# Optimization experiments

Hardware: AMD Instinct MI355X
Metric: run time of the kernel (lower is better)

Reference implementation:

```python
import jax, jax.numpy as jnp
import numpy as np

B, OBS, ACT, NT, E, H1, H2, D = 4096, 390, 20, 10, 8, 1024, 512, 256


def setup_inputs() -> dict:
    key = jax.random.key(0)
    ks = jax.random.split(key, 16)
    f32 = jnp.float32

    def w(k, shape, fan_in):
        return jax.random.normal(k, shape, f32) / np.float32(np.sqrt(fan_in))

    return {
        "state_feat": jax.random.normal(ks[0], (B, OBS), f32),
        "act": jax.random.normal(ks[1], (B, ACT), f32),
        "task_id": jax.random.randint(ks[2], (B,), 0, NT, jnp.int32),
        "rep_W1": w(ks[3], (OBS + ACT, H1), OBS + ACT),
        "rep_b1": jnp.zeros((H1,), f32),
        "rep_W2": w(ks[4], (H1, H1), H1),
        "rep_b2": jnp.zeros((H1,), f32),
        "emb": 0.5 * jax.random.normal(ks[5], (NT, D), f32),
        "kW1": w(ks[6], (E, H1, H2), H1),
        "kb1": jnp.zeros((E, H2), f32),
        "kW2": w(ks[7], (E, H2, D), H2),
        "kb2": jnp.zeros((E, D), f32),
        "vW1": w(ks[8], (E, H1, H2), H1),
        "vb1": jnp.zeros((E, H2), f32),
        "vW2": w(ks[9], (E, H2, D), H2),
        "vb2": jnp.zeros((E, D), f32),
        "tW1": w(ks[10], (D, D), D),
        "tb1": jnp.zeros((D,), f32),
        "tW2": w(ks[11], (D, D), D),
        "tb2": jnp.zeros((D,), f32),
        "tW3": w(ks[12], (D, 1), D),
        "tb3": jnp.zeros((1,), f32),
    }


def reference(state_feat, act, task_id, rep_W1, rep_b1, rep_W2, rep_b2, emb,
              kW1, kb1, kW2, kb2, vW1, vb1, vW2, vb2,
              tW1, tb1, tW2, tb2, tW3, tb3):
    # representation: mlp([obs+act, 1024, 1024]) -> ReLU on first layer only
    x = jnp.concatenate([state_feat, act], axis=-1)              # [B, 410]
    rep = jnp.maximum(x @ rep_W1 + rep_b1, 0.0) @ rep_W2 + rep_b2  # [B, H1]
    query = jnp.tanh(emb[task_id])                               # [B, D]

    # batched per-expert key/value MLPs (grouped GEMM instead of python loop)
    hk = jnp.maximum(jnp.einsum('bi,eio->ebo', rep, kW1) + kb1[:, None, :], 0.0)
    keys = jnp.einsum('ebo,eod->ebd', hk, kW2) + kb2[:, None, :]   # [E, B, D]
    hv = jnp.maximum(jnp.einsum('bi,eio->ebo', rep, vW1) + vb1[:, None, :], 0.0)
    vals = jnp.einsum('ebo,eod->ebd', hv, vW2) + vb2[:, None, :]   # [E, B, D]

    scores = jnp.einsum('bd,ebd->be', query, keys)               # [B, E]
    weight = jax.nn.softmax(scores, axis=1)                      # [B, E]
    tower_in = jnp.einsum('be,ebd->bd', weight, vals)            # [B, D]

    # tower: mlp([256, 256, 256, 1]) -> ReLU, ReLU, Identity
    h = jnp.maximum(tower_in @ tW1 + tb1, 0.0)
    h = jnp.maximum(h @ tW2 + tb2, 0.0)
    q = (h @ tW3 + tb3)[:, 0]                                    # [B]

    expert_loss = -jnp.mean(
        jnp.sum(jnp.clip(jnp.log(weight + 1e-10), -6.0, 0.0), axis=-1) * 0.3)
    return q, expert_loss
```

## Files before the change

kernel.cpp:

```cpp
#include <hip/hip_runtime.h>

constexpr int Bn   = 4096;
constexpr int OBS  = 390;
constexpr int ACTN = 20;
constexpr int IN   = 410;
constexpr int KPAD = 448;
constexpr int E    = 8;
constexpr int NT   = 10;
constexpr int H1   = 1024;
constexpr int H2   = 512;
constexpr int D    = 256;

typedef __bf16 bf16x8 __attribute__((ext_vector_type(8)));
typedef float  f32x4  __attribute__((ext_vector_type(4)));
typedef unsigned short u16x8 __attribute__((ext_vector_type(8)));

__device__ __forceinline__ unsigned short f2bf(float f) {
    unsigned int u = __float_as_uint(f);
    unsigned int r = u + 0x7fffu + ((u >> 16) & 1u);
    return (unsigned short)(r >> 16);
}
__device__ __forceinline__ float bf2f(unsigned short h) {
    return __uint_as_float(((unsigned int)h) << 16);
}
__device__ __forceinline__ void gload16(void* lds_dst, const void* g_src) {
    __builtin_amdgcn_global_load_lds(
        (const __attribute__((address_space(1))) void*)g_src,
        (__attribute__((address_space(3))) void*)lds_dst,
        16, 0, 0);
}

struct TD2 {
    const float* W;
    unsigned short* WT;
    int K, Kpad, N;
    long long gsW, gsO;
    int tilesN, perG, start;
};
struct TD2Arr { TD2 d[8]; };

__global__ __launch_bounds__(256) void tc64(TD2Arr da) {
    int bid = blockIdx.x;
    int i = 0;
#pragma unroll
    for (int j = 1; j < 8; ++j) if (bid >= da.d[j].start) i = j;
    TD2 dd = da.d[i];
    int local = bid - dd.start;
    int g   = local / dd.perG;
    int rem = local - g * dd.perG;
    int kt  = rem / dd.tilesN;
    int nt  = rem - kt * dd.tilesN;
    const float* W = dd.W + (long long)g * dd.gsW;
    unsigned short* WT = dd.WT + (long long)g * dd.gsO;
    int k0 = kt * 64, n0 = nt * 64;

    __shared__ float tile[64][68];
    int t = threadIdx.x;
    {
        int kl  = t >> 4;
        int nl4 = (t & 15) * 4;
#pragma unroll
        for (int r = 0; r < 4; ++r) {
            int k = k0 + kl + r * 16;
            float4 v = make_float4(0.f, 0.f, 0.f, 0.f);
            if (k < dd.K) v = *(const float4*)(W + (long long)k * dd.N + n0 + nl4);
            *(float4*)&tile[kl + r * 16][nl4] = v;
        }
    }
    __syncthreads();
    int nl = t >> 2, kc = (t & 3) * 16;
    if (k0 + kc < dd.Kpad) {
        u16x8 o0, o1;
#pragma unroll
        for (int j = 0; j < 8; ++j) {
            o0[j] = f2bf(tile[kc + j][nl]);
            o1[j] = f2bf(tile[kc + 8 + j][nl]);
        }
        unsigned short* dst = WT + (long long)(n0 + nl) * dd.Kpad + k0 + kc;
        *(u16x8*)dst       = o0;
        *(u16x8*)(dst + 8) = o1;
    }
}

constexpr int PREPB = (Bn * KPAD) / 256;

__global__ __launch_bounds__(256) void misc_kernel(
    const float* __restrict__ sf, const float* __restrict__ ac,
    unsigned short* __restrict__ x,
    const float* __restrict__ kW2, const float* __restrict__ kb2,
    const float* __restrict__ emb, float* __restrict__ qp, float* __restrict__ qb,
    const float* __restrict__ kb1, const float* __restrict__ vb1,
    float* __restrict__ b1cat)
{
    int bid = blockIdx.x;
    if (bid < PREPB) {
        int idx = bid * 256 + threadIdx.x;
        int b = idx / KPAD;
        int k = idx - b * KPAD;
        float v = 0.f;
        if (k < OBS) v = sf[b * OBS + k];
        else if (k < IN) v = ac[b * ACTN + (k - OBS)];
        x[idx] = f2bf(v);
        return;
    }
    if (bid < PREPB + 17) {
        int qbid = bid - PREPB;
        __shared__ float tq[NT][D];
        for (int i = threadIdx.x; i < NT * D; i += 256)
            tq[i / D][i - (i / D) * D] = tanhf(emb[i]);
        __syncthreads();
        if (qbid < 16) {
            int e = qbid >> 1;
            int h = (qbid & 1) * 256 + threadIdx.x;
            const float4* row = (const float4*)(kW2 + ((long long)e * H2 + h) * D);
            float acc[NT] = {};
            for (int d4 = 0; d4 < D / 4; ++d4) {
                float4 wv = row[d4];
#pragma unroll
                for (int t = 0; t < NT; ++t)
                    acc[t] += wv.x * tq[t][d4 * 4] + wv.y * tq[t][d4 * 4 + 1]
                            + wv.z * tq[t][d4 * 4 + 2] + wv.w * tq[t][d4 * 4 + 3];
            }
#pragma unroll
            for (int t = 0; t < NT; ++t)
                qp[((long long)e * NT + t) * H2 + h] = acc[t];
        } else if (threadIdx.x < E * NT) {
            int e = threadIdx.x / NT, t = threadIdx.x - e * NT;
            float s = 0.f;
            for (int d = 0; d < D; ++d) s += kb2[e * D + d] * tq[t][d];
            qb[e * NT + t] = s;
        }
        return;
    }
    int i = (bid - PREPB - 17) * 256 + threadIdx.x;
    b1cat[i] = (i < E * H2) ? kb1[i] : vb1[i - E * H2];
}

template <int KT, int ACTF, int OUTF>
__global__ __launch_bounds__(256, 2) void gemm128p(
    const unsigned short* __restrict__ A, const unsigned short* __restrict__ BT,
    const float* __restrict__ bias, void* __restrict__ Cout,
    int ldc, long long gsA, long long gsBT, long long gsBias, long long gsC,
    const float* __restrict__ tW3 = nullptr, float* __restrict__ qpart = nullptr)
{
    constexpr int NTK = KT / 64;
    static_assert(NTK >= 2, "KT must be >= 128");

    const int g = blockIdx.z;
    A    += (long long)g * gsA;
    BT   += (long long)g * gsBT;
    bias += (long long)g * gsBias;
    float*          Cf = (float*)Cout + (long long)g * gsC;
    unsigned short* Cb = (unsigned short*)Cout + (long long)g * gsC;

    __shared__ __align__(16) char smem[65536];
    const int tid = threadIdx.x;
    const int l  = tid & 63, lr = l & 15, lk = l >> 4;
    const int w  = tid >> 6;
    const int wm = (w >> 1) * 64, wn = (w & 1) * 64;
    const int gm = blockIdx.y * 128, gn = blockIdx.x * 128;

    const int srow = tid >> 3;
    const int cg   = (tid & 7) ^ (srow & 7);
    const unsigned short* gA = A  + (long long)(gm + srow) * KT + cg * 8;
    const unsigned short* gB = BT + (long long)(gn + srow) * KT + cg * 8;
    const int wb = w * 1024;

    const int cs0 = ((0 | lk) ^ (lr & 7)) * 16;
    const int cs1 = ((4 | lk) ^ (lr & 7)) * 16;
    const int aRow = (wm + lr) * 128;
    const int bRow = 16384 + (wn + lr) * 128;

    f32x4 acc[4][4] = {};

    auto stA = [&](int c, int kt) {
#pragma unroll
        for (int j = 0; j < 4; ++j)
            gload16(smem + c * 32768 + j * 4096 + wb,
                    gA + (long long)(j * 32) * KT + kt * 64);
    };
    auto stB = [&](int c, int kt) {
#pragma unroll
        for (int j = 0; j < 4; ++j)
            gload16(smem + c * 32768 + 16384 + j * 4096 + wb,
                    gB + (long long)(j * 32) * KT + kt * 64);
    };

    stA(0, 0); stB(0, 0); stA(1, 1);
    asm volatile("s_waitcnt vmcnt(4)" ::: "memory");
    __builtin_amdgcn_s_barrier();
    __builtin_amdgcn_sched_barrier(0);

#pragma unroll
    for (int kt = 0; kt < NTK; ++kt) {
        const int c = kt & 1;
        const char* bufc = smem + c * 32768;
        bf16x8 a[4][2], b[2][2], b2[2][2];

#pragma unroll
        for (int m = 0; m < 4; ++m) {
            const char* base = bufc + aRow + m * 2048;
            a[m][0] = *(const bf16x8*)(base + cs0);
            a[m][1] = *(const bf16x8*)(base + cs1);
        }
#pragma unroll
        for (int n = 0; n < 2; ++n) {
            const char* base = bufc + bRow + n * 2048;
            b[n][0] = *(const bf16x8*)(base + cs0);
            b[n][1] = *(const bf16x8*)(base + cs1);
        }
        if (kt + 1 < NTK) stB(c ^ 1, kt + 1);
        __builtin_amdgcn_s_setprio(1);
#pragma unroll
        for (int ks = 0; ks < 2; ++ks)
#pragma unroll
            for (int m = 0; m < 4; ++m)
#pragma unroll
                for (int n = 0; n < 2; ++n)
                    acc[m][n] = __builtin_amdgcn_mfma_f32_16x16x32_bf16(
                        a[m][ks], b[n][ks], acc[m][n], 0, 0, 0);
        __builtin_amdgcn_s_setprio(0);

#pragma unroll
        for (int n = 0; n < 2; ++n) {
            const char* base = bufc + bRow + (2 + n) * 2048;
            b2[n][0] = *(const bf16x8*)(base + cs0);
            b2[n][1] = *(const bf16x8*)(base + cs1);
        }
        asm volatile("s_waitcnt lgkmcnt(0)" ::: "memory");
        __builtin_amdgcn_sched_barrier(0);
        if (kt + 2 < NTK) {
            __builtin_amdgcn_s_barrier();
            __builtin_amdgcn_sched_barrier(0);
            stA(c, kt + 2);
        }
        __builtin_amdgcn_s_setprio(1);
#pragma unroll
        for (int ks = 0; ks < 2; ++ks)
#pragma unroll
            for (int m = 0; m < 4; ++m)
#pragma unroll
                for (int n = 0; n < 2; ++n)
                    acc[m][2 + n] = __builtin_amdgcn_mfma_f32_16x16x32_bf16(
                        a[m][ks], b2[n][ks], acc[m][2 + n], 0, 0, 0);
        __builtin_amdgcn_s_setprio(0);

        if (kt + 1 < NTK) {
            if (kt + 2 < NTK) { asm volatile("s_waitcnt vmcnt(4)" ::: "memory"); }
            else              { asm volatile("s_waitcnt vmcnt(0)" ::: "memory"); }
            __builtin_amdgcn_sched_barrier(0);
            __builtin_amdgcn_s_barrier();
            __builtin_amdgcn_sched_barrier(0);
        }
    }

    const int orow0 = gm + wm + lk * 4;
    const int ocol0 = gn + wn + lr;
    float bv[4];
#pragma unroll
    for (int ni = 0; ni < 4; ++ni) bv[ni] = bias[gn + wn + lr + ni * 16];

    if (OUTF == 2) {
        float tw3v[4];
#pragma unroll
        for (int ni = 0; ni < 4; ++ni) tw3v[ni] = tW3[gn + wn + lr + ni * 16];
#pragma unroll
        for (int mi = 0; mi < 4; ++mi)
#pragma unroll
            for (int r = 0; r < 4; ++r) {
                float part = 0.f;
#pragma unroll
                for (int ni = 0; ni < 4; ++ni) {
                    float v = acc[mi][ni][r] + bv[ni];
                    if (ACTF == 1) v = fmaxf(v, 0.f);
                    part += v * tw3v[ni];
                }
                part += __shfl_xor(part, 1);
                part += __shfl_xor(part, 2);
                part += __shfl_xor(part, 4);
                part += __shfl_xor(part, 8);
                if (lr == 0)
                    qpart[(orow0 + mi * 16 + r) * 4 + ((wn >> 6) << 1) + blockIdx.x] = part;
            }
    } else {
#pragma unroll
        for (int mi = 0; mi < 4; ++mi)
#pragma unroll
            for (int ni = 0; ni < 4; ++ni)
#pragma unroll
                for (int r = 0; r < 4; ++r) {
                    float v = acc[mi][ni][r] + bv[ni];
                    if (ACTF == 1) v = fmaxf(v, 0.f);
                    long long off = (long long)(orow0 + mi * 16 + r) * ldc + ocol0 + ni * 16;
                    if (OUTF == 0) Cf[off] = v;
                    else           Cb[off] = f2bf(v);
                }
    }
}

template <int KTOT, int ACTF, int OUTF, int SC>
__global__ __launch_bounds__(512, 2) void gemm256(
    const unsigned short* __restrict__ A, const unsigned short* __restrict__ BT,
    const float* __restrict__ bias, void* __restrict__ Cout,
    int ldc, long long gsA, long long gsBT, long long gsBias, long long gsC,
    const int* __restrict__ task_id, const float* __restrict__ qp,
    float* __restrict__ spart)
{
    constexpr int NT_ = KTOT / 64;
    static_assert(NT_ >= 4 && (NT_ % 2) == 0, "KTOT must be multiple of 128");

    const int g = blockIdx.z;
    A    += (long long)g * gsA;
    BT   += (long long)g * gsBT;
    bias += (long long)g * gsBias;
    float*          Cf = (float*)Cout + (long long)g * gsC;
    unsigned short* Cb = (unsigned short*)Cout + (long long)g * gsC;

    __shared__ __align__(16) char smem[131072];

    const int tid = threadIdx.x;
    const int l  = tid & 63;
    const int lr = l & 15, lk = l >> 4;
    const int w  = tid >> 6;
    const int wr = w >> 2, wc = w & 3;
    const int gm = blockIdx.y * 256, gn = blockIdx.x * 256;

    const int srow = tid >> 3;
    const int cg   = (tid & 7) ^ (srow & 7);
    const unsigned short* gA = A  + (long long)(gm + srow) * KTOT + cg * 8;
    const unsigned short* gB = BT + (long long)(gn + srow) * KTOT + cg * 8;
    const int wbase = (tid & ~63) * 16;

    const int cs0 = ((0 | lk) ^ (lr & 7)) * 16;
    const int cs1 = ((4 | lk) ^ (lr & 7)) * 16;
    const int aRow = wr * 16384 + lr * 128;
    const int bRow = 32768 + (wc >> 1) * 16384 + ((wc & 1) * 64 + lr) * 128;

    f32x4 acc[8][4] = {};

    auto stA = [&](int c, int s, int kt) {
        const unsigned short* src = gA + (long long)(s * 128) * KTOT + kt * 64;
        char* d = smem + c * 65536 + s * 16384 + wbase;
        gload16(d,        src);
        gload16(d + 8192, src + (long long)64 * KTOT);
    };
    auto stB = [&](int c, int s, int kt) {
        const unsigned short* src = gB + (long long)(s * 128) * KTOT + kt * 64;
        char* d = smem + c * 65536 + 32768 + s * 16384 + wbase;
        gload16(d,        src);
        gload16(d + 8192, src + (long long)64 * KTOT);
    };

    stA(0, 0, 0); stA(0, 1, 0); stB(0, 0, 0); stB(0, 1, 0);
    stA(1, 0, 1); stA(1, 1, 1);
    asm volatile("s_waitcnt vmcnt(4)" ::: "memory");
    __builtin_amdgcn_s_barrier();
    __builtin_amdgcn_sched_barrier(0);

#pragma unroll
    for (int kt = 0; kt < NT_; ++kt) {
        const int c = kt & 1;
        const char* bufc = smem + c * 65536;
        bf16x8 a0[4], a1[4], b0[4], b1[4];

#pragma unroll
        for (int m = 0; m < 4; ++m) {
            const char* base = bufc + aRow + m * (16 * 128);
            a0[m] = *(const bf16x8*)(base + cs0);
            a1[m] = *(const bf16x8*)(base + cs1);
        }
#pragma unroll
        for (int n = 0; n < 4; ++n) {
            const char* base = bufc + bRow + n * (16 * 128);
            b0[n] = *(const bf16x8*)(base + cs0);
            b1[n] = *(const bf16x8*)(base + cs1);
        }
        if (kt + 1 < NT_) { stB(c ^ 1, 0, kt + 1); stB(c ^ 1, 1, kt + 1); }
        __builtin_amdgcn_s_setprio(1);
#pragma unroll
        for (int m = 0; m < 4; ++m)
#pragma unroll
            for (int n = 0; n < 4; ++n) {
                acc[m][n] = __builtin_amdgcn_mfma_f32_16x16x32_bf16(a0[m], b0[n], acc[m][n], 0, 0, 0);
                acc[m][n] = __builtin_amdgcn_mfma_f32_16x16x32_bf16(a1[m], b1[n], acc[m][n], 0, 0, 0);
            }
        __builtin_amdgcn_s_setprio(0);

#pragma unroll
        for (int m = 0; m < 4; ++m) {
            const char* base = bufc + aRow + (64 + m * 16) * 128;
            a0[m] = *(const bf16x8*)(base + cs0);
            a1[m] = *(const bf16x8*)(base + cs1);
        }
        asm volatile("s_waitcnt lgkmcnt(0)" ::: "memory");
        __builtin_amdgcn_sched_barrier(0);
        if (kt + 2 < NT_) {
            __builtin_amdgcn_s_barrier();
            __builtin_amdgcn_sched_barrier(0);
            stA(c, 0, kt + 2); stA(c, 1, kt + 2);
        }
        __builtin_amdgcn_s_setprio(1);
#pragma unroll
        for (int m = 0; m < 4; ++m)
#pragma unroll
            for (int n = 0; n < 4; ++n) {
                acc[4 + m][n] = __builtin_amdgcn_mfma_f32_16x16x32_bf16(a0[m], b0[n], acc[4 + m][n], 0, 0, 0);
                acc[4 + m][n] = __builtin_amdgcn_mfma_f32_16x16x32_bf16(a1[m], b1[n], acc[4 + m][n], 0, 0, 0);
            }
        __builtin_amdgcn_s_setprio(0);

        if (kt + 1 < NT_) {
            if (kt + 2 < NT_) { asm volatile("s_waitcnt vmcnt(4)" ::: "memory"); }
            else              { asm volatile("s_waitcnt vmcnt(0)" ::: "memory"); }
            __builtin_amdgcn_sched_barrier(0);
            __builtin_amdgcn_s_barrier();
            __builtin_amdgcn_sched_barrier(0);
        }
    }

    const int orow0 = gm + wr * 128 + lk * 4;
    const int ocol0 = gn + wc * 64 + lr;
    float bv[4];
#pragma unroll
    for (int ni = 0; ni < 4; ++ni) bv[ni] = bias[gn + wc * 64 + lr + ni * 16];

    if (SC && g < E) {
        __syncthreads();
        float* qpl  = (float*)smem;
        int*   tidl = (int*)(smem + NT * 256 * 4);
        for (int i = tid; i < NT * 256; i += 512) {
            int tt = i >> 8, cc = i & 255;
            qpl[i] = qp[((long long)(g * NT + tt)) * H2 + gn + cc];
        }
        if (tid < 256) tidl[tid] = task_id[gm + tid];
        __syncthreads();

        const int rbase = wr * 128 + lk * 4;
        const int cbase = wc * 64 + lr;
#pragma unroll
        for (int mi = 0; mi < 8; ++mi) {
#pragma unroll
            for (int r = 0; r < 4; ++r) {
                int trow = tidl[rbase + mi * 16 + r];
                float rp = 0.f;
#pragma unroll
                for (int ni = 0; ni < 4; ++ni) {
                    float v = acc[mi][ni][r] + bv[ni];
                    v = fmaxf(v, 0.f);
                    rp += v * qpl[trow * 256 + cbase + ni * 16];
                }
                rp += __shfl_xor(rp, 1);
                rp += __shfl_xor(rp, 2);
                rp += __shfl_xor(rp, 4);
                rp += __shfl_xor(rp, 8);
                if (lr == 0)
                    spart[(((long long)g * Bn + orow0 + mi * 16 + r) << 3)
                          + (wc << 1) + blockIdx.x] = rp;
            }
        }
    } else {
#pragma unroll
        for (int mi = 0; mi < 8; ++mi)
#pragma unroll
            for (int ni = 0; ni < 4; ++ni)
#pragma unroll
                for (int r = 0; r < 4; ++r) {
                    float v = acc[mi][ni][r] + bv[ni];
                    if (ACTF == 1) v = fmaxf(v, 0.f);
                    long long off = (long long)(orow0 + mi * 16 + r) * ldc + ocol0 + ni * 16;
                    if (OUTF == 0) Cf[off] = v;
                    else           Cb[off] = f2bf(v);
                }
    }
}

__global__ __launch_bounds__(256) void attn_kernel(
    const float* __restrict__ spart, const float* __restrict__ qb,
    const int* __restrict__ task_id, const unsigned short* __restrict__ vals,
    unsigned short* __restrict__ tower_in, float* __restrict__ loss_partial)
{
    int wv   = threadIdx.x >> 6;
    int lane = threadIdx.x & 63;
    int b    = blockIdx.x * 4 + wv;
    int t    = task_id[b];

    float s[E];
#pragma unroll
    for (int e = 0; e < E; ++e) {
        const float4* sp = (const float4*)(spart + (((long long)e * Bn + b) << 3));
        float4 p0 = sp[0], p1 = sp[1];
        s[e] = p0.x + p0.y + p0.z + p0.w + p1.x + p1.y + p1.z + p1.w + qb[e * NT + t];
    }

    float m = s[0];
#pragma unroll
    for (int e = 1; e < E; ++e) m = fmaxf(m, s[e]);
    float wgt[E];
    float sum = 0.f;
#pragma unroll
    for (int e = 0; e < E; ++e) { wgt[e] = expf(s[e] - m); sum += wgt[e]; }
    float inv = 1.f / sum;

    int d0 = lane * 4;
    float4 acc = make_float4(0.f, 0.f, 0.f, 0.f);
    float lb = 0.f;
#pragma unroll
    for (int e = 0; e < E; ++e) {
        float we = wgt[e] * inv;
        uint2 vv = *(const uint2*)&vals[((long long)e * Bn + b) * D + d0];
        acc.x += we * __uint_as_float(vv.x << 16);
        acc.y += we * __uint_as_float(vv.x & 0xffff0000u);
        acc.z += we * __uint_as_float(vv.y << 16);
        acc.w += we * __uint_as_float(vv.y & 0xffff0000u);
        lb += fminf(fmaxf(logf(we + 1e-10f), -6.f), 0.f);
    }
    ushort4 o;
    o.x = f2bf(acc.x); o.y = f2bf(acc.y); o.z = f2bf(acc.z); o.w = f2bf(acc.w);
    *(ushort4*)&tower_in[(long long)b * D + d0] = o;

    __shared__ float sm[4];
    if (lane == 0) sm[wv] = lb;
    __syncthreads();
    if (threadIdx.x == 0)
        loss_partial[blockIdx.x] = sm[0] + sm[1] + sm[2] + sm[3];
}

__global__ __launch_bounds__(256) void qfin_kernel(
    const float* __restrict__ qpart, const float* __restrict__ tb3,
    float* __restrict__ out, const float* __restrict__ lossp)
{
    if (blockIdx.x == Bn / 256) {
        float s = 0.f;
        for (int i = threadIdx.x; i < Bn / 4; i += 256) s += lossp[i];
#pragma unroll
        for (int off = 32; off > 0; off >>= 1) s += __shfl_xor(s, off, 64);
        __shared__ float sm[4];
        if ((threadIdx.x & 63) == 0) sm[threadIdx.x >> 6] = s;
        __syncthreads();
        if (threadIdx.x == 0) out[Bn] = (-0.3f / Bn) * (sm[0] + sm[1] + sm[2] + sm[3]);
        return;
    }
    int b = blockIdx.x * 256 + threadIdx.x;
    float4 qpv = *(const float4*)&qpart[b * 4];
    out[b] = qpv.x + qpv.y + qpv.z + qpv.w + tb3[0];
}

extern "C" void kernel_launch(void* const* d_in, const int* in_sizes, int n_in,
                              void* d_out, int out_size, void* d_ws, size_t ws_size,
                              hipStream_t stream) {
    const float* state_feat = (const float*)d_in[0];
    const float* act        = (const float*)d_in[1];
    const int*   task_id    = (const int*)d_in[2];
    const float* rep_W1 = (const float*)d_in[3];
    const float* rep_b1 = (const float*)d_in[4];
    const float* rep_W2 = (const float*)d_in[5];
    const float* rep_b2 = (const float*)d_in[6];
    const float* emb    = (const float*)d_in[7];
    const float* kW1 = (const float*)d_in[8];
    const float* kb1 = (const float*)d_in[9];
    const float* kW2 = (const float*)d_in[10];
    const float* kb2 = (const float*)d_in[11];
    const float* vW1 = (const float*)d_in[12];
    const float* vb1 = (const float*)d_in[13];
    const float* vW2 = (const float*)d_in[14];
    const float* vb2 = (const float*)d_in[15];
    const float* tW1 = (const float*)d_in[16];
    const float* tb1 = (const float*)d_in[17];
    const float* tW2 = (const float*)d_in[18];
    const float* tb2 = (const float*)d_in[19];
    const float* tW3 = (const float*)d_in[20];
    const float* tb3 = (const float*)d_in[21];
    float* out = (float*)d_out;

    char* p = (char*)d_ws;
    auto alloc = [&](size_t bytes) {
        char* r = p;
        p += (bytes + 255) & ~(size_t)255;
        return r;
    };
    unsigned short* x      = (unsigned short*)alloc((size_t)Bn * KPAD * 2);
    unsigned short* repW1T = (unsigned short*)alloc((size_t)H1 * KPAD * 2);
    unsigned short* repW2T = (unsigned short*)alloc((size_t)H1 * H1 * 2);
    unsigned short* w1T    = (unsigned short*)alloc((size_t)2 * E * H2 * H1 * 2);
    unsigned short* w2T    = (unsigned short*)alloc((size_t)E * D * H2 * 2);
    unsigned short* tW1T   = (unsigned short*)alloc((size_t)D * D * 2);
    unsigned short* tW2T   = (unsigned short*)alloc((size_t)D * D * 2);
    float*          b1cat  = (float*)alloc((size_t)2 * E * H2 * 4);
    float*          qp     = (float*)alloc((size_t)E * NT * H2 * 4);
    float*          qb     = (float*)alloc((size_t)E * NT * 4);
    char*           h1zone = alloc((size_t)Bn * H1 * 2);
    unsigned short* rep    = (unsigned short*)alloc((size_t)Bn * H1 * 2);
    unsigned short* hkv    = (unsigned short*)alloc((size_t)2 * E * Bn * H2 * 2);
    unsigned short* vals   = (unsigned short*)alloc((size_t)E * Bn * D * 2);
    float*          spart  = (float*)alloc((size_t)E * Bn * 8 * 4);
    float*          qpart  = (float*)alloc((size_t)Bn * 4 * 4);
    float*          lossp  = (float*)alloc((size_t)(Bn / 4) * 4);

    unsigned short* h1       = (unsigned short*)h1zone;
    unsigned short* tower_in = (unsigned short*)h1zone;
    unsigned short* t1       = (unsigned short*)(h1zone + (size_t)Bn * D * 2);
    unsigned short* hv = hkv + (size_t)E * Bn * H2;

    TD2Arr da;
    int startAcc = 0;
    auto setd = [&](int i, const float* W, unsigned short* WT, int K, int Kpad, int N,
                    long long gsW, long long gsO, int groups) {
        TD2& dd = da.d[i];
        dd.W = W; dd.WT = WT; dd.K = K; dd.Kpad = Kpad; dd.N = N;
        dd.gsW = gsW; dd.gsO = gsO;
        dd.tilesN = N / 64;
        dd.perG = ((Kpad + 63) / 64) * dd.tilesN;
        dd.start = startAcc;
        startAcc += dd.perG * groups;
    };
    setd(0, rep_W1, repW1T, IN, KPAD, H1, 0, 0, 1);
    setd(1, rep_W2, repW2T, H1, H1, H1, 0, 0, 1);
    setd(2, kW1, w1T,                       H1, H1, H2, (long long)H1 * H2, (long long)H2 * H1, E);
    setd(3, vW1, w1T + (size_t)E * H2 * H1, H1, H1, H2, (long long)H1 * H2, (long long)H2 * H1, E);
    setd(4, vW2, w2T,                       H2, H2, D, (long long)H2 * D, (long long)D * H2, E);
    setd(5, tW1, tW1T, D, D, D, 0, 0, 1);
    setd(6, tW2, tW2T, D, D, D, 0, 0, 1);
    da.d[7] = da.d[6];
    da.d[7].start = 0x7fffffff;
    tc64<<<startAcc, 256, 0, stream>>>(da);

    misc_kernel<<<PREPB + 17 + 32, 256, 0, stream>>>(
        state_feat, act, x, kW2, kb2, emb, qp, qb, kb1, vb1, b1cat);

    gemm128p<KPAD, 1, 1><<<dim3(H1 / 128, Bn / 128, 1), 256, 0, stream>>>(
        x, repW1T, rep_b1, h1, H1, 0, 0, 0, 0);
    gemm128p<H1, 0, 1><<<dim3(H1 / 128, Bn / 128, 1), 256, 0, stream>>>(
        h1, repW2T, rep_b2, rep, H1, 0, 0, 0, 0);

    gemm256<H1, 1, 1, 1><<<dim3(H2 / 256, Bn / 256, 2 * E), 512, 0, stream>>>(
        rep, w1T, b1cat, hkv, H2,
        0, (long long)H2 * H1, H2, (long long)Bn * H2,
        task_id, qp, spart);
    gemm128p<H2, 0, 1><<<dim3(D / 128, Bn / 128, E), 256, 0, stream>>>(
        hv, w2T, vb2, vals, D,
        (long long)Bn * H2, (long long)D * H2, D, (long long)Bn * D);

    attn_kernel<<<Bn / 4, 256, 0, stream>>>(
        spart, qb, task_id, vals, tower_in, lossp);

    gemm128p<D, 1, 1><<<dim3(D / 128, Bn / 128, 1), 256, 0, stream>>>(
        tower_in, tW1T, tb1, t1, D, 0, 0, 0, 0);
    gemm128p<D, 1, 2><<<dim3(D / 128, Bn / 128, 1), 256, 0, stream>>>(
        t1, tW2T, tb2, nullptr, D, 0, 0, 0, 0, tW3, qpart);

    qfin_kernel<<<Bn / 256 + 1, 256, 0, stream>>>(qpart, tb3, out, lossp);
}
```

Before: 162.3 us.

## Restructure GEMM main loop into four A-subtile phases with interleaved prefetch

The k-loop of the grouped GEMM is split into four phases, each loading two 16-row A fragments and issuing their MFMAs, while B fragments are held in registers for the whole k-tile. Prefetch order is swapped: B is now staged one tile ahead and A is loaded into the alternate buffer in halves across phases. Smaller A register sets are meant to cut register pressure and spread global loads more evenly between MFMA bursts. The cost is many more workgroup barriers per iteration, which could stall waves.

```diff
diff --git a/kernel.cpp b/kernel.cpp
--- a/kernel.cpp
+++ b/kernel.cpp
@@ -352,7 +352,7 @@
     };
 
     stA(0, 0, 0); stA(0, 1, 0); stB(0, 0, 0); stB(0, 1, 0);
-    stA(1, 0, 1); stA(1, 1, 1);
+    stB(1, 0, 1); stB(1, 1, 1);
     asm volatile("s_waitcnt vmcnt(4)" ::: "memory");
     __builtin_amdgcn_s_barrier();
     __builtin_amdgcn_sched_barrier(0);
@@ -361,61 +361,107 @@
     for (int kt = 0; kt < NT_; ++kt) {
         const int c = kt & 1;
         const char* bufc = smem + c * 65536;
-        bf16x8 a0[4], a1[4], b0[4], b1[4];
-
-#pragma unroll
-        for (int m = 0; m < 4; ++m) {
-            const char* base = bufc + aRow + m * (16 * 128);
-            a0[m] = *(const bf16x8*)(base + cs0);
-            a1[m] = *(const bf16x8*)(base + cs1);
-        }
+        bf16x8 b[4][2], ap[2][2];
+
 #pragma unroll
         for (int n = 0; n < 4; ++n) {
-            const char* base = bufc + bRow + n * (16 * 128);
-            b0[n] = *(const bf16x8*)(base + cs0);
-            b1[n] = *(const bf16x8*)(base + cs1);
-        }
-        if (kt + 1 < NT_) { stB(c ^ 1, 0, kt + 1); stB(c ^ 1, 1, kt + 1); }
-        __builtin_amdgcn_s_setprio(1);
-#pragma unroll
-        for (int m = 0; m < 4; ++m)
-#pragma unroll
-            for (int n = 0; n < 4; ++n) {
-                acc[m][n] = __builtin_amdgcn_mfma_f32_16x16x32_bf16(a0[m], b0[n], acc[m][n], 0, 0, 0);
-                acc[m][n] = __builtin_amdgcn_mfma_f32_16x16x32_bf16(a1[m], b1[n], acc[m][n], 0, 0, 0);
-            }
-        __builtin_amdgcn_s_setprio(0);
-
-#pragma unroll
-        for (int m = 0; m < 4; ++m) {
-            const char* base = bufc + aRow + (64 + m * 16) * 128;
-            a0[m] = *(const bf16x8*)(base + cs0);
-            a1[m] = *(const bf16x8*)(base + cs1);
-        }
+            const char* base = bufc + bRow + n * 2048;
+            b[n][0] = *(const bf16x8*)(base + cs0);
+            b[n][1] = *(const bf16x8*)(base + cs1);
+        }
+#pragma unroll
+        for (int m = 0; m < 2; ++m) {
+            const char* base = bufc + aRow + m * 2048;
+            ap[m][0] = *(const bf16x8*)(base + cs0);
+            ap[m][1] = *(const bf16x8*)(base + cs1);
+        }
+        if (kt + 1 < NT_) stA(c ^ 1, 0, kt + 1);
+        __builtin_amdgcn_s_barrier();
         asm volatile("s_waitcnt lgkmcnt(0)" ::: "memory");
         __builtin_amdgcn_sched_barrier(0);
-        if (kt + 2 < NT_) {
-            __builtin_amdgcn_s_barrier();
-            __builtin_amdgcn_sched_barrier(0);
-            stA(c, 0, kt + 2); stA(c, 1, kt + 2);
-        }
         __builtin_amdgcn_s_setprio(1);
 #pragma unroll
-        for (int m = 0; m < 4; ++m)
-#pragma unroll
-            for (int n = 0; n < 4; ++n) {
-                acc[4 + m][n] = __builtin_amdgcn_mfma_f32_16x16x32_bf16(a0[m], b0[n], acc[4 + m][n], 0, 0, 0);
-                acc[4 + m][n] = __builtin_amdgcn_mfma_f32_16x16x32_bf16(a1[m], b1[n], acc[4 + m][n], 0, 0, 0);
-            }
+        for (int ks = 0; ks < 2; ++ks)
+#pragma unroll
+            for (int m = 0; m < 2; ++m)
+#pragma unroll
+                for (int n = 0; n < 4; ++n)
+                    acc[m][n] = __builtin_amdgcn_mfma_f32_16x16x32_bf16(
+                        ap[m][ks], b[n][ks], acc[m][n], 0, 0, 0);
         __builtin_amdgcn_s_setprio(0);
-
+        __builtin_amdgcn_s_barrier();
+
+#pragma unroll
+        for (int m = 0; m < 2; ++m) {
+            const char* base = bufc + aRow + 4096 + m * 2048;
+            ap[m][0] = *(const bf16x8*)(base + cs0);
+            ap[m][1] = *(const bf16x8*)(base + cs1);
+        }
+        if (kt + 1 < NT_) stA(c ^ 1, 1, kt + 1);
+        __builtin_amdgcn_s_barrier();
+        asm volatile("s_waitcnt lgkmcnt(0)" ::: "memory");
+        __builtin_amdgcn_sched_barrier(0);
+        __builtin_amdgcn_s_setprio(1);
+#pragma unroll
+        for (int ks = 0; ks < 2; ++ks)
+#pragma unroll
+            for (int m = 0; m < 2; ++m)
+#pragma unroll
+                for (int n = 0; n < 4; ++n)
+                    acc[2 + m][n] = __builtin_amdgcn_mfma_f32_16x16x32_bf16(
+                        ap[m][ks], b[n][ks], acc[2 + m][n], 0, 0, 0);
+        __builtin_amdgcn_s_setprio(0);
+        __builtin_amdgcn_s_barrier();
+
+#pragma unroll
+        for (int m = 0; m < 2; ++m) {
+            const char* base = bufc + aRow + 8192 + m * 2048;
+            ap[m][0] = *(const bf16x8*)(base + cs0);
+            ap[m][1] = *(const bf16x8*)(base + cs1);
+        }
+        if (kt + 2 < NT_) stB(c, 0, kt + 2);
+        __builtin_amdgcn_s_barrier();
+        asm volatile("s_waitcnt lgkmcnt(0)" ::: "memory");
+        __builtin_amdgcn_sched_barrier(0);
+        __builtin_amdgcn_s_setprio(1);
+#pragma unroll
+        for (int ks = 0; ks < 2; ++ks)
+#pragma unroll
+            for (int m = 0; m < 2; ++m)
+#pragma unroll
+                for (int n = 0; n < 4; ++n)
+                    acc[4 + m][n] = __builtin_amdgcn_mfma_f32_16x16x32_bf16(
+                        ap[m][ks], b[n][ks], acc[4 + m][n], 0, 0, 0);
+        __builtin_amdgcn_s_setprio(0);
+        __builtin_amdgcn_s_barrier();
+
+#pragma unroll
+        for (int m = 0; m < 2; ++m) {
+            const char* base = bufc + aRow + 12288 + m * 2048;
+            ap[m][0] = *(const bf16x8*)(base + cs0);
+            ap[m][1] = *(const bf16x8*)(base + cs1);
+        }
+        if (kt + 2 < NT_) stB(c, 1, kt + 2);
+        __builtin_amdgcn_s_barrier();
+        asm volatile("s_waitcnt lgkmcnt(0)" ::: "memory");
+        __builtin_amdgcn_sched_barrier(0);
+        __builtin_amdgcn_s_setprio(1);
+#pragma unroll
+        for (int ks = 0; ks < 2; ++ks)
+#pragma unroll
+            for (int m = 0; m < 2; ++m)
+#pragma unroll
+                for (int n = 0; n < 4; ++n)
+                    acc[6 + m][n] = __builtin_amdgcn_mfma_f32_16x16x32_bf16(
+                        ap[m][ks], b[n][ks], acc[6 + m][n], 0, 0, 0);
+        __builtin_amdgcn_s_setprio(0);
         if (kt + 1 < NT_) {
             if (kt + 2 < NT_) { asm volatile("s_waitcnt vmcnt(4)" ::: "memory"); }
             else              { asm volatile("s_waitcnt vmcnt(0)" ::: "memory"); }
             __builtin_amdgcn_sched_barrier(0);
-            __builtin_amdgcn_s_barrier();
-            __builtin_amdgcn_sched_barrier(0);
-        }
+        }
+        __builtin_amdgcn_s_barrier();
+        __builtin_amdgcn_sched_barrier(0);
     }
 
     const int orow0 = gm + wr * 128 + lk * 4;
```

Result: no change. 163.6 us (+0.8%).

## Merge prep kernels and use 64x128 tiles for representation GEMMs

Applied to the files above, without the earlier changes.

Fuses the weight transpose/convert kernel and the misc prep kernel into a single launch, removing one kernel launch and its tail. The two representation GEMMs switch from a 128x128 tile to a new 64x128 tile kernel with 3 blocks per CU, doubling the grid (512 blocks) to improve CU occupancy on the 256-CU device. The smaller tile lowers per-block data reuse, so operand traffic from L2 goes up.

```diff
diff --git a/kernel.cpp b/kernel.cpp
--- a/kernel.cpp
+++ b/kernel.cpp
@@ -39,52 +39,10 @@
 };
 struct TD2Arr { TD2 d[8]; };
 
-__global__ __launch_bounds__(256) void tc64(TD2Arr da) {
-    int bid = blockIdx.x;
-    int i = 0;
-#pragma unroll
-    for (int j = 1; j < 8; ++j) if (bid >= da.d[j].start) i = j;
-    TD2 dd = da.d[i];
-    int local = bid - dd.start;
-    int g   = local / dd.perG;
-    int rem = local - g * dd.perG;
-    int kt  = rem / dd.tilesN;
-    int nt  = rem - kt * dd.tilesN;
-    const float* W = dd.W + (long long)g * dd.gsW;
-    unsigned short* WT = dd.WT + (long long)g * dd.gsO;
-    int k0 = kt * 64, n0 = nt * 64;
-
-    __shared__ float tile[64][68];
-    int t = threadIdx.x;
-    {
-        int kl  = t >> 4;
-        int nl4 = (t & 15) * 4;
-#pragma unroll
-        for (int r = 0; r < 4; ++r) {
-            int k = k0 + kl + r * 16;
-            float4 v = make_float4(0.f, 0.f, 0.f, 0.f);
-            if (k < dd.K) v = *(const float4*)(W + (long long)k * dd.N + n0 + nl4);
-            *(float4*)&tile[kl + r * 16][nl4] = v;
-        }
-    }
-    __syncthreads();
-    int nl = t >> 2, kc = (t & 3) * 16;
-    if (k0 + kc < dd.Kpad) {
-        u16x8 o0, o1;
-#pragma unroll
-        for (int j = 0; j < 8; ++j) {
-            o0[j] = f2bf(tile[kc + j][nl]);
-            o1[j] = f2bf(tile[kc + 8 + j][nl]);
-        }
-        unsigned short* dst = WT + (long long)(n0 + nl) * dd.Kpad + k0 + kc;
-        *(u16x8*)dst       = o0;
-        *(u16x8*)(dst + 8) = o1;
-    }
-}
-
 constexpr int PREPB = (Bn * KPAD) / 256;
 
-__global__ __launch_bounds__(256) void misc_kernel(
+__global__ __launch_bounds__(256) void prep_all(
+    TD2Arr da, int tcb,
     const float* __restrict__ sf, const float* __restrict__ ac,
     unsigned short* __restrict__ x,
     const float* __restrict__ kW2, const float* __restrict__ kb2,
@@ -92,9 +50,52 @@
     const float* __restrict__ kb1, const float* __restrict__ vb1,
     float* __restrict__ b1cat)
 {
+    __shared__ float tile[64][68];
     int bid = blockIdx.x;
-    if (bid < PREPB) {
-        int idx = bid * 256 + threadIdx.x;
+    int t = threadIdx.x;
+
+    if (bid < tcb) {
+        int i = 0;
+#pragma unroll
+        for (int j = 1; j < 8; ++j) if (bid >= da.d[j].start) i = j;
+        TD2 dd = da.d[i];
+        int local = bid - dd.start;
+        int g   = local / dd.perG;
+        int rem = local - g * dd.perG;
+        int kt  = rem / dd.tilesN;
+        int nt  = rem - kt * dd.tilesN;
+        const float* W = dd.W + (long long)g * dd.gsW;
+        unsigned short* WT = dd.WT + (long long)g * dd.gsO;
+        int k0 = kt * 64, n0 = nt * 64;
+        {
+            int kl  = t >> 4;
+            int nl4 = (t & 15) * 4;
+#pragma unroll
+            for (int r = 0; r < 4; ++r) {
+                int k = k0 + kl + r * 16;
+                float4 v = make_float4(0.f, 0.f, 0.f, 0.f);
+                if (k < dd.K) v = *(const float4*)(W + (long long)k * dd.N + n0 + nl4);
+                *(float4*)&tile[kl + r * 16][nl4] = v;
+            }
+        }
+        __syncthreads();
+        int nl = t >> 2, kc = (t & 3) * 16;
+        if (k0 + kc < dd.Kpad) {
+            u16x8 o0, o1;
+#pragma unroll
+            for (int j = 0; j < 8; ++j) {
+                o0[j] = f2bf(tile[kc + j][nl]);
+                o1[j] = f2bf(tile[kc + 8 + j][nl]);
+            }
+            unsigned short* dst = WT + (long long)(n0 + nl) * dd.Kpad + k0 + kc;
+            *(u16x8*)dst       = o0;
+            *(u16x8*)(dst + 8) = o1;
+        }
+        return;
+    }
+    int bid2 = bid - tcb;
+    if (bid2 < PREPB) {
+        int idx = bid2 * 256 + t;
         int b = idx / KPAD;
         int k = idx - b * KPAD;
         float v = 0.f;
@@ -103,36 +104,35 @@
         x[idx] = f2bf(v);
         return;
     }
-    if (bid < PREPB + 17) {
-        int qbid = bid - PREPB;
-        __shared__ float tq[NT][D];
-        for (int i = threadIdx.x; i < NT * D; i += 256)
-            tq[i / D][i - (i / D) * D] = tanhf(emb[i]);
+    if (bid2 < PREPB + 17) {
+        int qbid = bid2 - PREPB;
+        float* tq = &tile[0][0];
+        for (int i = t; i < NT * D; i += 256) tq[i] = tanhf(emb[i]);
         __syncthreads();
         if (qbid < 16) {
             int e = qbid >> 1;
-            int h = (qbid & 1) * 256 + threadIdx.x;
+            int h = (qbid & 1) * 256 + t;
             const float4* row = (const float4*)(kW2 + ((long long)e * H2 + h) * D);
             float acc[NT] = {};
             for (int d4 = 0; d4 < D / 4; ++d4) {
                 float4 wv = row[d4];
 #pragma unroll
-                for (int t = 0; t < NT; ++t)
-                    acc[t] += wv.x * tq[t][d4 * 4] + wv.y * tq[t][d4 * 4 + 1]
-                            + wv.z * tq[t][d4 * 4 + 2] + wv.w * tq[t][d4 * 4 + 3];
+                for (int tt = 0; tt < NT; ++tt)
+                    acc[tt] += wv.x * tq[tt * D + d4 * 4] + wv.y * tq[tt * D + d4 * 4 + 1]
+                             + wv.z * tq[tt * D + d4 * 4 + 2] + wv.w * tq[tt * D + d4 * 4 + 3];
             }
 #pragma unroll
-            for (int t = 0; t < NT; ++t)
-                qp[((long long)e * NT + t) * H2 + h] = acc[t];
-        } else if (threadIdx.x < E * NT) {
-            int e = threadIdx.x / NT, t = threadIdx.x - e * NT;
+            for (int tt = 0; tt < NT; ++tt)
+                qp[((long long)e * NT + tt) * H2 + h] = acc[tt];
+        } else if (t < E * NT) {
+            int e = t / NT, tt = t - e * NT;
             float s = 0.f;
-            for (int d = 0; d < D; ++d) s += kb2[e * D + d] * tq[t][d];
-            qb[e * NT + t] = s;
+            for (int d = 0; d < D; ++d) s += kb2[e * D + d] * tq[tt * D + d];
+            qb[e * NT + tt] = s;
         }
         return;
     }
-    int i = (bid - PREPB - 17) * 256 + threadIdx.x;
+    int i = (bid2 - PREPB - 17) * 256 + t;
     b1cat[i] = (i < E * H2) ? kb1[i] : vb1[i - E * H2];
 }
 
@@ -296,6 +296,135 @@
                     else           Cb[off] = f2bf(v);
                 }
     }
+}
+
+template <int KT, int ACTF, int OUTF>
+__global__ __launch_bounds__(256, 3) void gemm64x128(
+    const unsigned short* __restrict__ A, const unsigned short* __restrict__ BT,
+    const float* __restrict__ bias, void* __restrict__ Cout,
+    int ldc, long long gsA, long long gsBT, long long gsBias, long long gsC)
+{
+    constexpr int NTK = KT / 64;
+    static_assert(NTK >= 2, "KT must be >= 128");
+
+    const int g = blockIdx.z;
+    A    += (long long)g * gsA;
+    BT   += (long long)g * gsBT;
+    bias += (long long)g * gsBias;
+    float*          Cf = (float*)Cout + (long long)g * gsC;
+    unsigned short* Cb = (unsigned short*)Cout + (long long)g * gsC;
+
+    __shared__ __align__(16) char smem[49152];
+    const int tid = threadIdx.x;
+    const int l  = tid & 63, lr = l & 15, lk = l >> 4;
+    const int w  = tid >> 6;
+    const int gm = blockIdx.y * 64, gn = blockIdx.x * 128;
+
+    const int srow = tid >> 3;
+    const int cg   = (tid & 7) ^ (srow & 7);
+    const unsigned short* gA = A  + (long long)(gm + srow) * KT + cg * 8;
+    const unsigned short* gB = BT + (long long)(gn + srow) * KT + cg * 8;
+    const int wb = w * 1024;
+
+    const int cs0 = ((0 | lk) ^ (lr & 7)) * 16;
+    const int cs1 = ((4 | lk) ^ (lr & 7)) * 16;
+    const int aRow = lr * 128;
+    const int bRow = 8192 + (w * 32 + lr) * 128;
+
+    f32x4 acc[4][2] = {};
+
+    auto stA = [&](int c, int kt) {
+#pragma unroll
+        for (int j = 0; j < 2; ++j)
+            gload16(smem + c * 24576 + j * 4096 + wb,
+                    gA + (long long)(j * 32) * KT + kt * 64);
+    };
+    auto stB = [&](int c, int kt) {
+#pragma unroll
+        for (int j = 0; j < 4; ++j)
+            gload16(smem + c * 24576 + 8192 + j * 4096 + wb,
+                    gB + (long long)(j * 32) * KT + kt * 64);
+    };
+
+    stA(0, 0); stB(0, 0); stA(1, 1);
+    asm volatile("s_waitcnt vmcnt(2)" ::: "memory");
+    __builtin_amdgcn_s_barrier();
+    __builtin_amdgcn_sched_barrier(0);
+
+#pragma unroll
+    for (int kt = 0; kt < NTK; ++kt) {
+        const int c = kt & 1;
+        const char* bufc = smem + c * 24576;
+        bf16x8 a[4][2], b[1][2], b2[1][2];
+
+#pragma unroll
+        for (int m = 0; m < 4; ++m) {
+            const char* base = bufc + aRow + m * 2048;
+            a[m][0] = *(const bf16x8*)(base + cs0);
+            a[m][1] = *(const bf16x8*)(base + cs1);
+        }
+        {
+            const char* base = bufc + bRow;
+            b[0][0] = *(const bf16x8*)(base + cs0);
+            b[0][1] = *(const bf16x8*)(base + cs1);
+        }
+        if (kt + 1 < NTK) stB(c ^ 1, kt + 1);
+        __builtin_amdgcn_s_setprio(1);
+#pragma unroll
+        for (int ks = 0; ks < 2; ++ks)
+#pragma unroll
+            for (int m = 0; m < 4; ++m)
+                acc[m][0] = __builtin_amdgcn_mfma_f32_16x16x32_bf16(
+                    a[m][ks], b[0][ks], acc[m][0], 0, 0, 0);
+        __builtin_amdgcn_s_setprio(0);
+
+        {
+            const char* base = bufc + bRow + 2048;
+            b2[0][0] = *(const bf16x8*)(base + cs0);
+            b2[0][1] = *(const bf16x8*)(base + cs1);
+        }
+        asm volatile("s_waitcnt lgkmcnt(0)" ::: "memory");
+        __builtin_amdgcn_sched_barrier(0);
+        if (kt + 2 < NTK) {
+            __builtin_amdgcn_s_barrier();
+            __builtin_amdgcn_sched_barrier(0);
+            stA(c, kt + 2);
+        }
+        __builtin_amdgcn_s_setprio(1);
+#pragma unroll
+        for (int ks = 0; ks < 2; ++ks)
+#pragma unroll
+            for (int m = 0; m < 4; ++m)
+                acc[m][1] = __builtin_amdgcn_mfma_f32_16x16x32_bf16(
+                    a[m][ks], b2[0][ks], acc[m][1], 0, 0, 0);
+        __builtin_amdgcn_s_setprio(0);
+
+        if (kt + 1 < NTK) {
+            if (kt + 2 < NTK) { asm volatile("s_waitcnt vmcnt(2)" ::: "memory"); }
+            else              { asm volatile("s_waitcnt vmcnt(0)" ::: "memory"); }
+            __builtin_amdgcn_sched_barrier(0);
+            __builtin_amdgcn_s_barrier();
+            __builtin_amdgcn_sched_barrier(0);
+        }
+    }
+
+    const int orow0 = gm + lk * 4;
+    const int ocol0 = gn + w * 32 + lr;
+    float bv[2];
+#pragma unroll
+    for (int nf = 0; nf < 2; ++nf) bv[nf] = bias[gn + w * 32 + lr + nf * 16];
+#pragma unroll
+    for (int mi = 0; mi < 4; ++mi)
+#pragma unroll
+        for (int nf = 0; nf < 2; ++nf)
+#pragma unroll
+            for (int r = 0; r < 4; ++r) {
+                float v = acc[mi][nf][r] + bv[nf];
+                if (ACTF == 1) v = fmaxf(v, 0.f);
+                long long off = (long long)(orow0 + mi * 16 + r) * ldc + ocol0 + nf * 16;
+                if (OUTF == 0) Cf[off] = v;
+                else           Cb[off] = f2bf(v);
+            }
 }
 
 template <int KTOT, int ACTF, int OUTF, int SC>
@@ -622,14 +751,13 @@
     setd(6, tW2, tW2T, D, D, D, 0, 0, 1);
     da.d[7] = da.d[6];
     da.d[7].start = 0x7fffffff;
-    tc64<<<startAcc, 256, 0, stream>>>(da);
-
-    misc_kernel<<<PREPB + 17 + 32, 256, 0, stream>>>(
-        state_feat, act, x, kW2, kb2, emb, qp, qb, kb1, vb1, b1cat);
-
-    gemm128p<KPAD, 1, 1><<<dim3(H1 / 128, Bn / 128, 1), 256, 0, stream>>>(
+    int totalBlocks = startAcc + PREPB + 17 + 32;
+    prep_all<<<totalBlocks, 256, 0, stream>>>(
+        da, startAcc, state_feat, act, x, kW2, kb2, emb, qp, qb, kb1, vb1, b1cat);
+
+    gemm64x128<KPAD, 1, 1><<<dim3(H1 / 128, Bn / 64, 1), 256, 0, stream>>>(
         x, repW1T, rep_b1, h1, H1, 0, 0, 0, 0);
-    gemm128p<H1, 0, 1><<<dim3(H1 / 128, Bn / 128, 1), 256, 0, stream>>>(
+    gemm64x128<H1, 0, 1><<<dim3(H1 / 128, Bn / 64, 1), 256, 0, stream>>>(
         h1, repW2T, rep_b2, rep, H1, 0, 0, 0, 0);
 
     gemm256<H1, 1, 1, 1><<<dim3(H2 / 256, Bn / 256, 2 * E), 512, 0, stream>>>(
```

New measurement: 159.8 us. Within noise of the previous version (-1.5%).
